# Kernel optimization log

Measured on AMD Instinct MI355X. Metric: run time of the kernel, lower is better.

## Reference

```python
import jax, jax.numpy as jnp
import numpy as np
from jax import lax

B, T, C, U = 32, 512, 4233, 64


def setup_inputs() -> dict:
    key = jax.random.key(0)
    k1, k2 = jax.random.split(key)
    logits = jax.random.normal(k1, (B, T, C), dtype=jnp.float32)
    ctc_logit = jax.nn.log_softmax(logits, axis=-1)  # [B, T, C] log-probs
    # labels in [1, C) so none equal blank (code treats blank-valued labels as pad)
    label = jax.random.randint(k2, (U, B), 1, C, dtype=jnp.int32)  # [U, B]
    return {"ctc_logit": ctc_logit, "label": label, "blank_id": 0}


def ctc_fa(ctc_logit, label, blank_id):
    pad_value = jnp.finfo(ctc_logit.dtype).min
    lab = label.T  # [B, U]
    lab = jnp.where(lab == blank_id, -1, lab)
    Bb, Uu = lab.shape
    Tt = ctc_logit.shape[1]
    Cc = ctc_logit.shape[2]
    yl = (lab >= 0).sum(1) * 2 + 1  # [B] extended label length
    # interleave blanks: [blank, l0, blank, l1, ..., blank] -> lab_T = 2U+1
    blanks = jnp.full_like(lab, blank_id)
    ext = jnp.stack([blanks, lab], axis=2).reshape(Bb, 2 * Uu)
    ext = jnp.pad(ext, ((0, 0), (0, 1)), constant_values=blank_id)  # [B, labT]
    labT = 2 * Uu + 1
    shifted2 = jnp.pad(ext, ((0, 0), (2, 0)), constant_values=-1)[:, :labT]
    cond = (ext == blank_id) | (ext == shifted2)  # [B, labT]
    ext_idx = ext % Cc  # mimic torch negative-index wrap for -1 pad labels
    # emission log-probs gathered per extended-label position: [B, T, labT]
    emit = jnp.take_along_axis(ctc_logit, ext_idx[:, None, :], axis=2)
    dp0 = jnp.full((Bb, labT), pad_value, ctc_logit.dtype)
    dp0 = dp0.at[:, 0].set(emit[:, 0, 0]).at[:, 1].set(emit[:, 0, 1])
    jrange = jnp.arange(labT)

    def shift(x, n):
        return jnp.pad(x, ((0, 0), (n, 0)), constant_values=pad_value)[:, :labT]

    def step(dp_prev, emit_t):
        s1 = shift(dp_prev, 1)
        s2 = shift(dp_prev, 2)
        a2 = jnp.stack([dp_prev, s1], axis=-1)          # [B, labT, 2]
        a3 = jnp.stack([dp_prev, s1, s2], axis=-1)      # [B, labT, 3]
        idx1 = jnp.argmax(a2, axis=-1)
        idx2 = jnp.argmax(a3, axis=-1)
        lse2 = jax.scipy.special.logsumexp(a2, axis=-1)
        lse3 = jax.scipy.special.logsumexp(a3, axis=-1)
        dp_t = emit_t + jnp.where(cond, lse2, lse3)
        bp_t = jrange[None, :] - jnp.where(cond, idx1, idx2)
        return dp_t, (dp_t, bp_t)

    emit_tbj = jnp.swapaxes(emit, 0, 1)  # [T, B, labT]
    dp_last, (_, bps) = lax.scan(step, dp0, emit_tbj[1:])
    bp0 = jnp.broadcast_to(jrange[None, None, :], (1, Bb, labT)).astype(bps.dtype)
    bp_all = jnp.concatenate([bp0, bps], axis=0)  # [T, B, labT]
    bi = jnp.arange(Bb)
    d1 = dp_last[bi, yl - 1]
    d2 = dp_last[bi, yl - 2]
    ctc_loss = -jnp.logaddexp(d1, d2)
    ctc_loss = 2 * ctc_loss / (yl - 1)
    # Viterbi backtrack -> hard alignment [B, T, labT]
    wi0 = jnp.where(d1 > d2, yl - 1, yl - 2)

    def bstep(wi, bp_t):
        align_t = (jrange[None, :] == wi[:, None]).astype(jnp.int32)
        wi_next = jnp.take_along_axis(bp_t, wi[:, None], axis=1)[:, 0]
        return wi_next, align_t

    _, align_ts = lax.scan(bstep, wi0, bp_all, reverse=True)  # [T, B, labT]
    align = jnp.swapaxes(align_ts, 0, 1)  # [B, T, labT]
    return align, ctc_loss


def reference(ctc_logit, label, blank_id):
    return ctc_fa(ctc_logit, label, blank_id)
```

## Files before the change

### kernel.cpp

```cpp
#include <hip/hip_runtime.h>
#include <math.h>

#define NB 32
#define NT 512
#define NC 4233
#define NU 64
#define LABT 129
#define PADV (-3.4028234663852886e38f)
#define EMIT_N (NB * NT * LABT)

__global__ __launch_bounds__(256)
void ctc_gather_kernel(const float* __restrict__ logit,
                       const int*   __restrict__ label,
                       const int*   __restrict__ blank_ptr,
                       float*       __restrict__ emitP,
                       float*       __restrict__ emitL)
{
    int tid = blockIdx.x * 256 + threadIdx.x;
    if (tid >= EMIT_N) return;
    int bt = tid / LABT;
    int j  = tid - bt * LABT;
    int b  = bt / NT;
    int blank = blank_ptr[0];
    int col;
    if (j & 1) {
        int raw = label[((j - 1) >> 1) * NB + b];
        int ev  = (raw == blank) ? -1 : raw;
        col = ev % NC;
        if (col < 0) col += NC;
    } else {
        col = blank;
    }
    float v = logit[(size_t)bt * NC + col];
    if (j < 128) emitP[(size_t)bt * 128 + j] = v;
    else         emitL[bt] = v;
}

__global__ __launch_bounds__(64)
void ctc_scan_kernel(const float* __restrict__ emitP,
                     const float* __restrict__ emitL,
                     const int*   __restrict__ label,
                     const int*   __restrict__ blank_ptr,
                     float* __restrict__ out,
                     float* __restrict__ loss_out)
{
    __shared__ __align__(16) unsigned long long bpm[NT][4];
    __shared__ int   wl[NT];
    __shared__ float fdp[132];

    const int b = blockIdx.x;
    const int l = threadIdx.x;
    const int blank = blank_ptr[0];

    int raw = label[l * NB + b];
    unsigned long long nbmask = __ballot(raw != blank);
    const int Y = 2 * (int)__popcll(nbmask) + 1;
    int ev  = (raw == blank) ? -1 : raw;
    int pev = __shfl_up(ev, 1);
    if (l == 0) pev = -1;
    const bool cndO = (ev == blank) || (ev == pev);

    const float2* ep = (const float2*)(emitP + (size_t)b * NT * 128) + l;
    const float*  el = emitL + (size_t)b * NT;

    float2 e00 = ep[0];
    float v0 = (l == 0) ? e00.x : PADV;
    float v1 = (l == 0) ? e00.y : PADV;
    float v2 = PADV;

    float2 r0 = ep[1 * 64], r1 = ep[2 * 64], r2 = ep[3 * 64], r3 = ep[4 * 64];
    float  q0 = el[1], q1 = el[2], q2 = el[3], q3 = el[4];

#define STEP(tcur, rr, qq, tload)                                              \
    do {                                                                       \
        float u1 = __shfl_up(v1, 1);                                           \
        u1 = (l == 0) ? PADV : u1;                               \
                              \
        float mE   = fmaxf(v0, u1);                                            \
        float lseE = mE + logf(1.0f + expf(-fabsf(v0 - u1)));                  \
        unsigned long long bE = __ballot(v0 < u1);                             \
                       \
        float c2e = cndO ? PADV : u1;                                          \
        float mO  = fmaxf(fmaxf(v1, v0), c2e);                                 \
        float lseO = mO + logf(expf(v1 - mO) + expf(v0 - mO) + expf(c2e - mO));\
        unsigned long long gAB = __ballot(v1 >= v0);                           \
        unsigned long long gAC = __ballot(v1 >= c2e);                          \
        unsigned long long gBC = __ballot(v0 >= c2e);                          \
                                    \
        float mL   = fmaxf(v2, v1);                                            \
        float lseL = mL + logf(1.0f + expf(-fabsf(v2 - v1)));                  \
        unsigned long long bL = __ballot(v2 < v1);                             \
        v0 = rr.x + lseE;                                                      \
        v1 = rr.y + lseO;                                                      \
        v2 = qq   + lseL;                                                      \
        if (l == 0) {                                                          \
            unsigned long long t0m = gAB & gAC;                                \
            bpm[tcur][0] = bE;                                                 \
            bpm[tcur][1] = ~t0m & gBC;                                         \
            bpm[tcur][2] = ~t0m & ~gBC;                                        \
            bpm[tcur][3] = (bL >> 63);                                         \
        }                                                                      \
        if ((tload) < NT) { rr = ep[(tload) * 64]; qq = el[(tload)]; }         \
    } while (0)

    int t = 1;
    for (; t + 3 < NT; t += 4) {
        STEP(t,     r0, q0, t + 4);
        STEP(t + 1, r1, q1, t + 5);
        STEP(t + 2, r2, q2, t + 6);
        STEP(t + 3, r3, q3, t + 7);
    }
    STEP(t,     r0, q0, NT);
    STEP(t + 1, r1, q1, NT);
    STEP(t + 2, r2, q2, NT);
#undef STEP

    fdp[2 * l]     = v0;
    fdp[2 * l + 1] = v1;
    if (l == 63) fdp[128] = v2;
    __syncthreads();

    float* outA = out + (size_t)b * (NT * LABT);
    {
        float4 z4; z4.x = 0.f; z4.y = 0.f; z4.z = 0.f; z4.w = 0.f;
        float4* o4 = (float4*)outA;
        for (int p = l; p < (NT * LABT) / 4; p += 64) o4[p] = z4;
    }

    if (l == 0) {
        int i2 = Y - 2; if (i2 < 0) i2 += LABT;
        float d1 = fdp[Y - 1];
        float d2 = fdp[i2];
        float mm = fmaxf(d1, d2);
        float la = mm + logf(expf(d1 - mm) + expf(d2 - mm));
        loss_out[b] = -la * 2.0f / (float)(Y - 1);

        int w = (d1 > d2) ? (Y - 1) : i2;
        const ulonglong2* bp2 = (const ulonglong2*)&bpm[0][0];

#define BLOAD(qa, qb, row) do { qa = bp2[2 * (row)]; qb = bp2[2 * (row) + 1]; } while (0)
#define BPROC(qa, qb, row) do {                                                \
        wl[row] = w;                                                           \
        int lw_ = w >> 1;                                                      \
        int dE_ = (w == 128) ? (int)qb.y : (int)((qa.x >> lw_) & 1ULL);        \
        int dO_ = (int)((qa.y >> lw_) & 1ULL) + 2 * (int)((qb.x >> lw_) & 1ULL);\
        w -= (w & 1) ? dO_ : dE_;                                              \
    } while (0)

        ulonglong2 a0, b0, a1, b1, a2, b2, a3, b3;
        BLOAD(a0, b0, NT - 1);
        BLOAD(a1, b1, NT - 2);
        BLOAD(a2, b2, NT - 3);
        BLOAD(a3, b3, NT - 4);
        int tt;
        for (tt = NT - 1; tt >= 8; tt -= 4) {
            BPROC(a0, b0, tt    ); BLOAD(a0, b0, tt - 4);
            BPROC(a1, b1, tt - 1); BLOAD(a1, b1, tt - 5);
            BPROC(a2, b2, tt - 2); BLOAD(a2, b2, tt - 6);
            BPROC(a3, b3, tt - 3); BLOAD(a3, b3, tt - 7);
        }
        BPROC(a0, b0, 7); BLOAD(a0, b0, 3);
        BPROC(a1, b1, 6); BLOAD(a1, b1, 2);
        BPROC(a2, b2, 5); BLOAD(a2, b2, 1);
        BPROC(a3, b3, 4);
        BPROC(a0, b0, 3);
        BPROC(a1, b1, 2);
        BPROC(a2, b2, 1);
        wl[0] = w;
#undef BLOAD
#undef BPROC
    }
    __syncthreads();

    for (int t2 = l; t2 < NT; t2 += 64)
        outA[(size_t)t2 * LABT + wl[t2]] = 1.0f;
}

extern "C" void kernel_launch(void* const* d_in, const int* in_sizes, int n_in,
                              void* d_out, int out_size, void* d_ws, size_t ws_size,
                              hipStream_t stream)
{
    const float* logit = (const float*)d_in[0];
    const int*   label = (const int*)d_in[1];
    const int*   blank = (const int*)d_in[2];

    float* out = (float*)d_out;

    float* emitP = (float*)d_ws;
    float* emitL = emitP + (size_t)NB * NT * 128;

    ctc_gather_kernel<<<(EMIT_N + 255) / 256, 256, 0, stream>>>(
        logit, label, blank, emitP, emitL);
    ctc_scan_kernel<<<NB, 64, 0, stream>>>(
        emitP, emitL, label, blank, out, out + (size_t)NB * NT * LABT);
}
```

Before: 566.9 us.

## Drop separate last-column emit buffer, use DPP shift and deeper prefetch

The final blank emission column is no longer gathered into its own buffer. It is read from lane 0's even-position value via readfirstlane, since every even extended position is the blank log-prob. The lane shift-up now uses a DPP wave_shr1 with PADV fill instead of __shfl_up plus a select, and the prefetch/unroll depth in the serial scan goes from 4 to 8 steps. The aim is to cut per-step latency on the serial dependency chain and remove the strided scalar loads of emitL. In exchange it uses more registers and assumes the DPP wave-shift control behaves correctly on this architecture.

```diff
diff --git a/kernel.cpp b/kernel.cpp
--- a/kernel.cpp
+++ b/kernel.cpp
@@ -7,19 +7,18 @@
 #define NU 64
 #define LABT 129
 #define PADV (-3.4028234663852886e38f)
-#define EMIT_N (NB * NT * LABT)
+#define EMITP_N (NB * NT * 128)
 
 __global__ __launch_bounds__(256)
 void ctc_gather_kernel(const float* __restrict__ logit,
                        const int*   __restrict__ label,
                        const int*   __restrict__ blank_ptr,
-                       float*       __restrict__ emitP,
-                       float*       __restrict__ emitL)
+                       float*       __restrict__ emitP)
 {
     int tid = blockIdx.x * 256 + threadIdx.x;
-    if (tid >= EMIT_N) return;
-    int bt = tid / LABT;
-    int j  = tid - bt * LABT;
+    if (tid >= EMITP_N) return;
+    int bt = tid >> 7;
+    int j  = tid & 127;
     int b  = bt / NT;
     int blank = blank_ptr[0];
     int col;
@@ -31,14 +30,17 @@
     } else {
         col = blank;
     }
-    float v = logit[(size_t)bt * NC + col];
-    if (j < 128) emitP[(size_t)bt * 128 + j] = v;
-    else         emitL[bt] = v;
+    emitP[tid] = logit[(size_t)bt * NC + col];
+}
+
+__device__ __forceinline__ float dpp_wave_shr1(float x, float fill) {
+    return __int_as_float(__builtin_amdgcn_update_dpp(
+        __float_as_int(fill), __float_as_int(x), 0x138 ,
+        0xf, 0xf, false));
 }
 
 __global__ __launch_bounds__(64)
 void ctc_scan_kernel(const float* __restrict__ emitP,
-                     const float* __restrict__ emitL,
                      const int*   __restrict__ label,
                      const int*   __restrict__ blank_ptr,
                      float* __restrict__ out,
@@ -61,7 +63,6 @@
     const bool cndO = (ev == blank) || (ev == pev);
 
     const float2* ep = (const float2*)(emitP + (size_t)b * NT * 128) + l;
-    const float*  el = emitL + (size_t)b * NT;
 
     float2 e00 = ep[0];
     float v0 = (l == 0) ? e00.x : PADV;
@@ -69,17 +70,16 @@
     float v2 = PADV;
 
     float2 r0 = ep[1 * 64], r1 = ep[2 * 64], r2 = ep[3 * 64], r3 = ep[4 * 64];
-    float  q0 = el[1], q1 = el[2], q2 = el[3], q3 = el[4];
-
-#define STEP(tcur, rr, qq, tload)                                              \
+    float2 r4 = ep[5 * 64], r5 = ep[6 * 64], r6 = ep[7 * 64], r7 = ep[8 * 64];
+
+#define STEP(tcur, rr, tload)                                                  \
     do {                                                                       \
-        float u1 = __shfl_up(v1, 1);                                           \
-        u1 = (l == 0) ? PADV : u1;                               \
+        float u1 = dpp_wave_shr1(v1, PADV);                      \
                               \
         float mE   = fmaxf(v0, u1);                                            \
         float lseE = mE + logf(1.0f + expf(-fabsf(v0 - u1)));                  \
         unsigned long long bE = __ballot(v0 < u1);                             \
-                       \
+                     \
         float c2e = cndO ? PADV : u1;                                          \
         float mO  = fmaxf(fmaxf(v1, v0), c2e);                                 \
         float lseO = mO + logf(expf(v1 - mO) + expf(v0 - mO) + expf(c2e - mO));\
@@ -90,9 +90,12 @@
         float mL   = fmaxf(v2, v1);                                            \
         float lseL = mL + logf(1.0f + expf(-fabsf(v2 - v1)));                  \
         unsigned long long bL = __ballot(v2 < v1);                             \
+                            \
+        float eL = __int_as_float(                                             \
+            __builtin_amdgcn_readfirstlane(__float_as_int(rr.x)));             \
         v0 = rr.x + lseE;                                                      \
         v1 = rr.y + lseO;                                                      \
-        v2 = qq   + lseL;                                                      \
+        v2 = eL   + lseL;                                                      \
         if (l == 0) {                                                          \
             unsigned long long t0m = gAB & gAC;                                \
             bpm[tcur][0] = bE;                                                 \
@@ -100,19 +103,27 @@
             bpm[tcur][2] = ~t0m & ~gBC;                                        \
             bpm[tcur][3] = (bL >> 63);                                         \
         }                                                                      \
-        if ((tload) < NT) { rr = ep[(tload) * 64]; qq = el[(tload)]; }         \
+        if ((tload) < NT) rr = ep[(tload) * 64];                               \
     } while (0)
 
     int t = 1;
-    for (; t + 3 < NT; t += 4) {
-        STEP(t,     r0, q0, t + 4);
-        STEP(t + 1, r1, q1, t + 5);
-        STEP(t + 2, r2, q2, t + 6);
-        STEP(t + 3, r3, q3, t + 7);
-    }
-    STEP(t,     r0, q0, NT);
-    STEP(t + 1, r1, q1, NT);
-    STEP(t + 2, r2, q2, NT);
+    for (; t + 7 < NT; t += 8) {
+        STEP(t,     r0, t + 8);
+        STEP(t + 1, r1, t + 9);
+        STEP(t + 2, r2, t + 10);
+        STEP(t + 3, r3, t + 11);
+        STEP(t + 4, r4, t + 12);
+        STEP(t + 5, r5, t + 13);
+        STEP(t + 6, r6, t + 14);
+        STEP(t + 7, r7, t + 15);
+    }
+    STEP(t,     r0, NT);
+    STEP(t + 1, r1, NT);
+    STEP(t + 2, r2, NT);
+    STEP(t + 3, r3, NT);
+    STEP(t + 4, r4, NT);
+    STEP(t + 5, r5, NT);
+    STEP(t + 6, r6, NT);
 #undef STEP
 
     fdp[2 * l]     = v0;
@@ -187,10 +198,9 @@
     float* out = (float*)d_out;
 
     float* emitP = (float*)d_ws;
-    float* emitL = emitP + (size_t)NB * NT * 128;
-
-    ctc_gather_kernel<<<(EMIT_N + 255) / 256, 256, 0, stream>>>(
-        logit, label, blank, emitP, emitL);
+
+    ctc_gather_kernel<<<EMITP_N / 256, 256, 0, stream>>>(
+        logit, label, blank, emitP);
     ctc_scan_kernel<<<NB, 64, 0, stream>>>(
-        emitP, emitL, label, blank, out, out + (size_t)NB * NT * LABT);
-}
+        emitP, label, blank, out, out + (size_t)NB * NT * LABT);
+}
```

Result: faster. 542.3 us (-4.3%).
